# Performance work log

Measured on AMD Instinct MI355X. Metric: run time of the kernel, lower is better.

Reference implementation:

```python
import jax, jax.numpy as jnp
import numpy as np

DN = ('NCH', 'OIH', 'NCH')

def conv1d(x, w, b, pad):
    y = jax.lax.conv_general_dilated(x, w, (1,), [(pad, pad)], dimension_numbers=DN)
    return y if b is None else y + b[None, :, None]

def bn_eval(x, g, b, m, v, eps):
    s = g * jax.lax.rsqrt(v + eps)
    return x * s[None, :, None] + (b - m * s)[None, :, None]

def swish(x):
    return x * jax.nn.sigmoid(x)

def setup_inputs() -> dict:
    key = jax.random.key(0)
    ks = jax.random.split(key, 8)
    B, T, P = 16, 8192, 32
    inp = {
        'x': jax.random.normal(ks[0], (B, 1, T), jnp.float32),
        'conv_w': jax.random.normal(ks[1], (512, 1, 9), jnp.float32) * 0.1,
        'bn_g': jnp.ones((512,), jnp.float32),
        'bn_b': jnp.zeros((512,), jnp.float32),
        'bn_m': jnp.zeros((512,), jnp.float32),
        'bn_v': jnp.ones((512,), jnp.float32),
        'p1_w': jax.random.normal(ks[2], (P, 2, 31), jnp.float32) * 0.1,
        'p1_b': jnp.zeros((P,), jnp.float32),
        'pbn1_g': jnp.ones((P,), jnp.float32),
        'pbn1_b': jnp.zeros((P,), jnp.float32),
        'pbn1_m': jnp.zeros((P,), jnp.float32),
        'pbn1_v': jnp.ones((P,), jnp.float32),
        'p2_w': jax.random.normal(ks[3], (P, P, 15), jnp.float32) * 0.05,
        'p2_b': jnp.zeros((P,), jnp.float32),
        'pbn2_g': jnp.ones((P,), jnp.float32),
        'pbn2_b': jnp.zeros((P,), jnp.float32),
        'pbn2_m': jnp.zeros((P,), jnp.float32),
        'pbn2_v': jnp.ones((P,), jnp.float32),
        'p3_w': jax.random.normal(ks[4], (2, P, 15), jnp.float32) * 0.001,  # source scales last conv weight by 0.01
        'p3_b': jnp.full((2,), -np.log(2.0), jnp.float32),                 # source sets bias to -log(2)
        'norm_mean': jnp.ones((1,), jnp.float32),                           # eval-mode renorm buffer
    }
    return inp

def reference(x, conv_w, bn_g, bn_b, bn_m, bn_v,
              p1_w, p1_b, pbn1_g, pbn1_b, pbn1_m, pbn1_v,
              p2_w, p2_b, pbn2_g, pbn2_b, pbn2_m, pbn2_v,
              p3_w, p3_b, norm_mean):
    B, _, T = x.shape
    # main conv -> BN(eps=1e-3) -> GLU(dim=1); dropout is identity in eval
    h = conv1d(x, conv_w, None, 9 // 2)                 # [B, 512, T]
    h = bn_eval(h, bn_g, bn_b, bn_m, bn_v, 1e-3)
    a, g = jnp.split(h, 2, axis=1)
    features = a * jax.nn.sigmoid(g)                    # [B, 256, T]
    # predictor on cat([x, x*x])
    j = conv1d(jnp.concatenate([x, x * x], axis=1), p1_w, p1_b, 15)
    j = swish(bn_eval(j, pbn1_g, pbn1_b, pbn1_m, pbn1_v, 1e-5))
    j = conv1d(j, p2_w, p2_b, 7)
    j = swish(bn_eval(j, pbn2_g, pbn2_b, pbn2_m, pbn2_v, 1e-5))
    j = conv1d(j, p3_w, p3_b, 7)                        # [B, 2, T]
    weights = jax.nn.sigmoid(j[:, 0, :])                # [B, T]
    moves = jax.nn.sigmoid(j[:, 1, :])
    bmoves = moves
    moves = moves * norm_mean[0]                        # eval: renorm = norm_mean buffer
    # CIF-style dynamic pooling (row_pool), vectorized over batch
    feats = jnp.transpose(features, (0, 2, 1))          # [B, T, C]
    fw = feats * weights[..., None]
    poses = jnp.cumsum(jax.lax.stop_gradient(moves), axis=1)  # moves.detach() in source
    floors = jnp.floor(poses)
    w1 = 1.0 - (poses - floors)
    w2 = poses - floors
    fl = floors.astype(jnp.int32)
    ce = fl + 1
    Lmax = T + 2  # static bound: poses <= T so ceil index <= T+1
    C = fw.shape[2]
    def pool(fw_i, fl_i, ce_i, w1_i, w2_i):
        out = jnp.zeros((Lmax, C), fw_i.dtype)
        out = out.at[fl_i].add(w1_i[:, None] * fw_i)
        out = out.at[ce_i].add(w2_i[:, None] * fw_i)
        return out
    x_evs = jax.vmap(pool)(fw, fl, ce, w1, w2)          # [B, Lmax, C]
    lens = fl[:, -1] + 2                                 # int(ceils[-1]) + 1
    x_evs = jnp.transpose(x_evs, (0, 2, 1))             # [B, C, Lmax]
    pad = 3 - (Lmax % 3)
    x_evs = jnp.pad(x_evs, ((0, 0), (0, 0), (0, pad)))
    return x_evs, lens, bmoves, weights
```

## Files before the change

kernel.cpp:

```cpp
#include <hip/hip_runtime.h>
#include <math.h>

static constexpr int TT = 8192;
static constexpr int LFULL = 8196;
static constexpr int BSTRIDE = LFULL + 2;

static constexpr size_t XE_OFF   = 0;
static constexpr size_t LENS_OFF = (size_t)16*256*LFULL;
static constexpr size_t BM_OFF   = LENS_OFF + 16;
static constexpr size_t WT_OFF   = BM_OFF + (size_t)16*TT;

static constexpr size_t U_OFF     = 0;
static constexpr size_t V_OFF     = U_OFF + (size_t)16*32*TT;
static constexpr size_t MOVES_OFF = V_OFF + (size_t)16*32*TT;
static constexpr size_t C1_OFF    = MOVES_OFF + (size_t)16*TT;
static constexpr size_t C2_OFF    = C1_OFF + (size_t)16*TT;
static constexpr size_t BND_OFF   = U_OFF;

__device__ __forceinline__ float sig_(float z) { return 1.0f / (1.0f + __expf(-z)); }

__global__ __launch_bounds__(256) void k_conv1(
    const float* __restrict__ x,
    const float* __restrict__ p1w, const float* __restrict__ p1b,
    const float* __restrict__ g1, const float* __restrict__ b1,
    const float* __restrict__ m1, const float* __restrict__ v1,
    float* __restrict__ u)
{
    __shared__ float xin[2 * 320];
    __shared__ float w1t[2 * 992];
    const int tid = threadIdx.x;
    const int b = blockIdx.y;
    const int t0 = blockIdx.x * 256;

    for (int idx = tid; idx < 640; idx += 256) {
        int ci = idx / 320, xl = idx - ci * 320;
        int id = t0 - 15 + xl;
        float val = 0.f;
        if (xl < 286 && id >= 0 && id < TT) val = x[b * TT + id];
        xin[idx] = ci ? val * val : val;
    }
    for (int idx = tid; idx < 1984; idx += 256) {
        int c = idx / 62; int r = idx - c * 62; int ci = r / 31; int k = r - ci * 31;
        w1t[ci * 992 + c * 31 + k] = p1w[idx];
    }
    __syncthreads();

    const int tg = tid >> 5, c = tid & 31;
    float acc[32];
    const float bias = p1b[c];
#pragma unroll
    for (int i = 0; i < 32; ++i) acc[i] = bias;

    for (int h = 0; h < 4; ++h) {
        for (int ci = 0; ci < 2; ++ci) {
            float win[40];
            const float4* wp = (const float4*)(&xin[ci * 320 + tg * 32 + h * 8]);
#pragma unroll
            for (int r = 0; r < 10; ++r) {
                float4 q = wp[r];
                win[4*r] = q.x; win[4*r+1] = q.y; win[4*r+2] = q.z; win[4*r+3] = q.w;
            }
#pragma unroll
            for (int k = 0; k < 31; ++k) {
                float w = w1t[ci * 992 + c * 31 + k];
#pragma unroll
                for (int i = 0; i < 8; ++i) acc[h*8+i] = fmaf(w, win[i + k], acc[h*8+i]);
            }
        }
    }
    const float s = g1[c] * rsqrtf(v1[c] + 1e-5f);
    const float sh = b1[c] - m1[c] * s;
    float* up = &u[((size_t)(b * 32 + c)) * TT + t0 + tg * 32];
#pragma unroll
    for (int i = 0; i < 8; ++i) {
        float z0 = fmaf(acc[4*i+0], s, sh);
        float z1 = fmaf(acc[4*i+1], s, sh);
        float z2 = fmaf(acc[4*i+2], s, sh);
        float z3 = fmaf(acc[4*i+3], s, sh);
        ((float4*)up)[i] = make_float4(z0 * sig_(z0), z1 * sig_(z1), z2 * sig_(z2), z3 * sig_(z3));
    }
}

__global__ __launch_bounds__(256) void k_conv2(
    const float* __restrict__ u,
    const float* __restrict__ p2w, const float* __restrict__ p2b,
    const float* __restrict__ g2, const float* __restrict__ b2,
    const float* __restrict__ m2, const float* __restrict__ v2,
    float* __restrict__ vout)
{
    __shared__ float uld[32 * 144];
    __shared__ float w2t[32 * 240];
    const int tid = threadIdx.x;
    const int b = blockIdx.y;
    const int t0 = blockIdx.x * 128;
    const int ch = blockIdx.z;

    for (int idx = tid; idx < 32 * 144; idx += 256) {
        int ci = idx / 144, tl = idx - ci * 144;
        int tg = t0 - 7 + tl;
        float val = 0.f;
        if (tl < 142 && tg >= 0 && tg < TT) val = u[((size_t)(b * 32 + ci)) * TT + tg];
        uld[idx] = val;
    }
    for (int idx = tid; idx < 32 * 240; idx += 256) {
        int ci = idx / 240; int r = idx - ci * 240; int cl = r / 15; int k = r - cl * 15;
        w2t[idx] = p2w[(ch * 16 + cl) * 480 + ci * 15 + k];
    }
    __syncthreads();

    const int tg = tid >> 4, cl = tid & 15;
    const int c = ch * 16 + cl;
    float acc[8];
    const float bias = p2b[c];
#pragma unroll
    for (int i = 0; i < 8; ++i) acc[i] = bias;

    for (int ci = 0; ci < 32; ++ci) {
        float win[24];
        const float4* wp = (const float4*)(&uld[ci * 144 + tg * 8]);
#pragma unroll
        for (int r = 0; r < 6; ++r) {
            float4 q = wp[r];
            win[4*r] = q.x; win[4*r+1] = q.y; win[4*r+2] = q.z; win[4*r+3] = q.w;
        }
#pragma unroll
        for (int k = 0; k < 15; ++k) {
            float w = w2t[ci * 240 + cl * 15 + k];
#pragma unroll
            for (int i = 0; i < 8; ++i) acc[i] = fmaf(w, win[i + k], acc[i]);
        }
    }
    const float s = g2[c] * rsqrtf(v2[c] + 1e-5f);
    const float sh = b2[c] - m2[c] * s;
    float o[8];
#pragma unroll
    for (int i = 0; i < 8; ++i) { float z = fmaf(acc[i], s, sh); o[i] = z * sig_(z); }
    float* vp = &vout[((size_t)(b * 32 + c)) * TT + t0 + tg * 8];
    ((float4*)vp)[0] = make_float4(o[0], o[1], o[2], o[3]);
    ((float4*)vp)[1] = make_float4(o[4], o[5], o[6], o[7]);
}

__global__ __launch_bounds__(256) void k_conv3(
    const float* __restrict__ vin,
    const float* __restrict__ p3w, const float* __restrict__ p3b,
    const float* __restrict__ nm,
    float* __restrict__ outw, float* __restrict__ outbm, float* __restrict__ moves)
{
    __shared__ float vld[32 * 272];
    const int tid = threadIdx.x;
    const int b = blockIdx.y;
    const int t0 = blockIdx.x * 256;

    for (int idx = tid; idx < 32 * 272; idx += 256) {
        int ci = idx / 272, tl = idx - ci * 272;
        int tg = t0 - 7 + tl;
        float val = 0.f;
        if (tl < 270 && tg >= 0 && tg < TT) val = vin[((size_t)(b * 32 + ci)) * TT + tg];
        vld[idx] = val;
    }
    __syncthreads();

    float a0 = p3b[0], a1 = p3b[1];
    for (int ci = 0; ci < 32; ++ci) {
        float win[15];
#pragma unroll
        for (int k = 0; k < 15; ++k) win[k] = vld[ci * 272 + tid + k];
#pragma unroll
        for (int k = 0; k < 15; ++k) {
            a0 = fmaf(p3w[ci * 15 + k], win[k], a0);
            a1 = fmaf(p3w[480 + ci * 15 + k], win[k], a1);
        }
    }
    const int t = t0 + tid;
    const float wt = sig_(a0);
    const float bm = sig_(a1);
    outw[b * TT + t] = wt;
    outbm[b * TT + t] = bm;
    moves[b * TT + t] = bm * nm[0];
}

__global__ __launch_bounds__(1024) void k_scan(
    const float* __restrict__ moves, const float* __restrict__ wts,
    float* __restrict__ coef1, float* __restrict__ coef2,
    int* __restrict__ bnd, float* __restrict__ lens)
{
    __shared__ float wsum[16];
    const int tid = threadIdx.x;
    const int b = blockIdx.x;
    const int lane = tid & 63, wv = tid >> 6;
    float carry = 0.f;

    int* bb = &bnd[b * BSTRIDE];
    for (int i = tid; i < BSTRIDE; i += 1024) bb[i] = TT;
    if (tid == 0) { bb[0] = 0; bb[1] = 0; }
    __syncthreads();

    const float4* mv4 = (const float4*)&moves[b * TT];
    const float4* wt4 = (const float4*)&wts[b * TT];
    float4* c14 = (float4*)&coef1[b * TT];
    float4* c24 = (float4*)&coef2[b * TT];

    for (int chunk = 0; chunk < 2; ++chunk) {
        const int idx = chunk * 1024 + tid;
        float4 m = mv4[idx];
        const float s = m.x + m.y + m.z + m.w;
        float v = s;
#pragma unroll
        for (int off = 1; off < 64; off <<= 1) {
            float n = __shfl_up(v, off, 64);
            if (lane >= off) v += n;
        }
        if (lane == 63) wsum[wv] = v;
        __syncthreads();
        float pre = carry;
        for (int w = 0; w < wv; ++w) pre += wsum[w];
        float tot = 0.f;
#pragma unroll
        for (int w = 0; w < 16; ++w) tot += wsum[w];
        const float base = pre + (v - s);
        const float p0 = base + m.x;
        const float p1 = p0 + m.y;
        const float p2 = p1 + m.z;
        const float p3 = p2 + m.w;
        const float4 w4 = wt4[idx];
        const float fr0 = p0 - floorf(p0), fr1 = p1 - floorf(p1);
        const float fr2 = p2 - floorf(p2), fr3 = p3 - floorf(p3);
        c14[idx] = make_float4((1.f - fr0) * w4.x, (1.f - fr1) * w4.y,
                               (1.f - fr2) * w4.z, (1.f - fr3) * w4.w);
        c24[idx] = make_float4(fr0 * w4.x, fr1 * w4.y, fr2 * w4.z, fr3 * w4.w);
        {
            int lf = (int)floorf(base) + 1;
            const int lfe = (int)floorf(p3);
            const int tbase = idx << 2;
            for (; lf <= lfe; ++lf) {
                const float lff = (float)lf;
                int t = tbase;
                if (p0 >= lff) { }
                else if (p1 >= lff) t += 1;
                else if (p2 >= lff) t += 2;
                else t += 3;
                if (lf + 1 < BSTRIDE) bb[lf + 1] = t;
            }
        }
        if (chunk == 1 && tid == 1023) lens[b] = floorf(p3) + 2.0f;
        carry += tot;
        __syncthreads();
    }
}

static constexpr int LTILE = 16;
static constexpr int CHK = 128;

__global__ __launch_bounds__(256) void k_pool(
    const float* __restrict__ x,
    const float* __restrict__ cw,
    const float* __restrict__ bng, const float* __restrict__ bnb,
    const float* __restrict__ bnm, const float* __restrict__ bnv,
    const float* __restrict__ coef1, const float* __restrict__ coef2,
    const int* __restrict__ bnd,
    float* __restrict__ xevs)
{
    __shared__ float out_lds[256 * 17];
    __shared__ float4 xl4[36];
    __shared__ float4 c1l4[CHK / 4], c2l4[CHK / 4];
    __shared__ int lbs[LTILE + 2];
    float* xl = (float*)xl4;
    float* c1l = (float*)c1l4;
    float* c2l = (float*)c2l4;

    const int tid = threadIdx.x;
    const int b = blockIdx.y;
    const int l0 = blockIdx.x * LTILE;
    const int LTa = min(LTILE, LFULL - l0);

    if (tid < LTa + 2) lbs[tid] = bnd[b * BSTRIDE + l0 + tid];
    __syncthreads();

    const int t_lo = lbs[0];
    const int t_hi = lbs[LTa + 1];
    const size_t rowbase = (size_t)b * 256 * LFULL + l0;

    if (t_lo >= t_hi) {
        const float4 z = make_float4(0.f, 0.f, 0.f, 0.f);
#pragma unroll
        for (int it = 0; it < 4; ++it) {
            int idx4 = it * 256 + tid;
            int cc = idx4 >> 2, q = (idx4 & 3) << 2;
            if (q < LTa)
                *(float4*)(&xevs[rowbase + (size_t)cc * LFULL + q]) = z;
        }
        return;
    }

    {
#pragma unroll
        for (int li = 0; li < 17; ++li) out_lds[tid * 17 + li] = 0.f;
    }

    const int c = tid;
    float wa[9], wg[9];
#pragma unroll
    for (int k = 0; k < 9; ++k) { wa[k] = cw[c * 9 + k]; wg[k] = cw[(c + 256) * 9 + k]; }
    const float sa = bng[c] * rsqrtf(bnv[c] + 1e-3f);
    const float sha = bnb[c] - bnm[c] * sa;
    const float sg = bng[c + 256] * rsqrtf(bnv[c + 256] + 1e-3f);
    const float shg = bnb[c + 256] - bnm[c + 256] * sg;

    const float* xg = &x[b * TT];
    const float* c1g = &coef1[b * TT];
    const float* c2g = &coef2[b * TT];

    float accA = 0.f, accB = 0.f;
    int j = 0;
    int nb = lbs[1];

    for (int cs = t_lo; cs < t_hi; cs += CHK) {
        const int ce = min(cs + CHK, t_hi);
        const int len = ce - cs;
        __syncthreads();
        for (int idx = tid; idx < len + 12; idx += 256) {
            int id = cs - 4 + idx;
            xl[idx] = (id >= 0 && id < TT) ? xg[id] : 0.f;
        }
        if (tid < len) { c1l[tid] = c1g[cs + tid]; c2l[tid] = c2g[cs + tid]; }
        __syncthreads();

        const int len4 = len >> 2;
        for (int g = 0; g < len4; ++g) {
            float4 A = xl4[g], Bq = xl4[g + 1], Cq = xl4[g + 2];
            float w[12] = {A.x, A.y, A.z, A.w, Bq.x, Bq.y, Bq.z, Bq.w, Cq.x, Cq.y, Cq.z, Cq.w};
            float f[4];
#pragma unroll
            for (int i = 0; i < 4; ++i) {
                float s0 = 0.f, s1 = 0.f;
#pragma unroll
                for (int k = 0; k < 9; ++k) { s0 = fmaf(wa[k], w[i + k], s0); s1 = fmaf(wg[k], w[i + k], s1); }
                const float av = fmaf(s0, sa, sha);
                const float gv = fmaf(s1, sg, shg);
                f[i] = av * sig_(gv);
            }
            float4 c1v = c1l4[g], c2v = c2l4[g];
            const float c1a[4] = {c1v.x, c1v.y, c1v.z, c1v.w};
            const float c2a[4] = {c2v.x, c2v.y, c2v.z, c2v.w};
            const int tb = cs + (g << 2);
#pragma unroll
            for (int i = 0; i < 4; ++i) {
                const int t = tb + i;
                while (t >= nb) {
                    int li = j - 1;
                    if (li >= 0 && li < LTa) out_lds[c * 17 + li] = accA;
                    accA = accB; accB = 0.f;
                    ++j;
                    nb = lbs[j + 1];
                }
                accA = fmaf(c1a[i], f[i], accA);
                accB = fmaf(c2a[i], f[i], accB);
            }
        }
        for (int t = cs + (len4 << 2); t < ce; ++t) {
            const int il = t - cs;
            float s0 = 0.f, s1 = 0.f;
#pragma unroll
            for (int k = 0; k < 9; ++k) { float xv = xl[il + k]; s0 = fmaf(wa[k], xv, s0); s1 = fmaf(wg[k], xv, s1); }
            const float av = fmaf(s0, sa, sha);
            const float gv = fmaf(s1, sg, shg);
            const float f0 = av * sig_(gv);
            while (t >= nb) {
                int li = j - 1;
                if (li >= 0 && li < LTa) out_lds[c * 17 + li] = accA;
                accA = accB; accB = 0.f;
                ++j;
                nb = lbs[j + 1];
            }
            accA = fmaf(c1l[il], f0, accA);
            accB = fmaf(c2l[il], f0, accB);
        }
    }
    {
        int li = j - 1;
        if (li >= 0 && li < LTa) out_lds[c * 17 + li] = accA;
    }
    __syncthreads();

#pragma unroll
    for (int it = 0; it < 4; ++it) {
        int idx4 = it * 256 + tid;
        int cc = idx4 >> 2, q = (idx4 & 3) << 2;
        if (q < LTa) {
            float4 o;
            o.x = out_lds[cc * 17 + q + 0];
            o.y = out_lds[cc * 17 + q + 1];
            o.z = out_lds[cc * 17 + q + 2];
            o.w = out_lds[cc * 17 + q + 3];
            *(float4*)(&xevs[rowbase + (size_t)cc * LFULL + q]) = o;
        }
    }
}

extern "C" void kernel_launch(void* const* d_in, const int* in_sizes, int n_in,
                              void* d_out, int out_size, void* d_ws, size_t ws_size,
                              hipStream_t stream) {
    (void)in_sizes; (void)n_in; (void)out_size; (void)ws_size;
    const float* x      = (const float*)d_in[0];
    const float* conv_w = (const float*)d_in[1];
    const float* bn_g   = (const float*)d_in[2];
    const float* bn_b   = (const float*)d_in[3];
    const float* bn_m   = (const float*)d_in[4];
    const float* bn_v   = (const float*)d_in[5];
    const float* p1_w   = (const float*)d_in[6];
    const float* p1_b   = (const float*)d_in[7];
    const float* pbn1_g = (const float*)d_in[8];
    const float* pbn1_b = (const float*)d_in[9];
    const float* pbn1_m = (const float*)d_in[10];
    const float* pbn1_v = (const float*)d_in[11];
    const float* p2_w   = (const float*)d_in[12];
    const float* p2_b   = (const float*)d_in[13];
    const float* pbn2_g = (const float*)d_in[14];
    const float* pbn2_b = (const float*)d_in[15];
    const float* pbn2_m = (const float*)d_in[16];
    const float* pbn2_v = (const float*)d_in[17];
    const float* p3_w   = (const float*)d_in[18];
    const float* p3_b   = (const float*)d_in[19];
    const float* nm     = (const float*)d_in[20];

    float* out = (float*)d_out;
    float* ws  = (float*)d_ws;
    float* u     = ws + U_OFF;
    float* v     = ws + V_OFF;
    float* moves = ws + MOVES_OFF;
    float* coef1 = ws + C1_OFF;
    float* coef2 = ws + C2_OFF;
    int*   bnd   = (int*)(ws + BND_OFF);
    float* xevs  = out + XE_OFF;
    float* lens  = out + LENS_OFF;
    float* bmv   = out + BM_OFF;
    float* wts   = out + WT_OFF;

    k_conv1<<<dim3(32, 16), 256, 0, stream>>>(x, p1_w, p1_b, pbn1_g, pbn1_b, pbn1_m, pbn1_v, u);
    k_conv2<<<dim3(64, 16, 2), 256, 0, stream>>>(u, p2_w, p2_b, pbn2_g, pbn2_b, pbn2_m, pbn2_v, v);
    k_conv3<<<dim3(32, 16), 256, 0, stream>>>(v, p3_w, p3_b, nm, wts, bmv, moves);
    k_scan<<<16, 1024, 0, stream>>>(moves, wts, coef1, coef2, bnd, lens);
    k_pool<<<dim3((LFULL + LTILE - 1) / LTILE, 16), 256, 0, stream>>>(
        x, conv_w, bn_g, bn_b, bn_m, bn_v, coef1, coef2, bnd, xevs);
}
```

Baseline: 376.8 us.

## Split conv2 LDS staging into halves and move tail zeroing into a dedicated kernel

```diff
diff --git a/kernel.cpp b/kernel.cpp
--- a/kernel.cpp
+++ b/kernel.cpp
@@ -88,26 +88,13 @@
     const float* __restrict__ m2, const float* __restrict__ v2,
     float* __restrict__ vout)
 {
-    __shared__ float uld[32 * 144];
-    __shared__ float w2t[32 * 240];
+    __shared__ float uld[16 * 144];
+    __shared__ float w2t[16 * 240];
     const int tid = threadIdx.x;
     const int b = blockIdx.y;
     const int t0 = blockIdx.x * 128;
     const int ch = blockIdx.z;
 
-    for (int idx = tid; idx < 32 * 144; idx += 256) {
-        int ci = idx / 144, tl = idx - ci * 144;
-        int tg = t0 - 7 + tl;
-        float val = 0.f;
-        if (tl < 142 && tg >= 0 && tg < TT) val = u[((size_t)(b * 32 + ci)) * TT + tg];
-        uld[idx] = val;
-    }
-    for (int idx = tid; idx < 32 * 240; idx += 256) {
-        int ci = idx / 240; int r = idx - ci * 240; int cl = r / 15; int k = r - cl * 15;
-        w2t[idx] = p2w[(ch * 16 + cl) * 480 + ci * 15 + k];
-    }
-    __syncthreads();
-
     const int tg = tid >> 4, cl = tid & 15;
     const int c = ch * 16 + cl;
     float acc[8];
@@ -115,19 +102,35 @@
 #pragma unroll
     for (int i = 0; i < 8; ++i) acc[i] = bias;
 
-    for (int ci = 0; ci < 32; ++ci) {
-        float win[24];
-        const float4* wp = (const float4*)(&uld[ci * 144 + tg * 8]);
-#pragma unroll
-        for (int r = 0; r < 6; ++r) {
-            float4 q = wp[r];
-            win[4*r] = q.x; win[4*r+1] = q.y; win[4*r+2] = q.z; win[4*r+3] = q.w;
-        }
-#pragma unroll
-        for (int k = 0; k < 15; ++k) {
-            float w = w2t[ci * 240 + cl * 15 + k];
-#pragma unroll
-            for (int i = 0; i < 8; ++i) acc[i] = fmaf(w, win[i + k], acc[i]);
+    for (int h = 0; h < 2; ++h) {
+        __syncthreads();
+        for (int idx = tid; idx < 16 * 144; idx += 256) {
+            int ci = idx / 144, tl = idx - ci * 144;
+            int tgl = t0 - 7 + tl;
+            float val = 0.f;
+            if (tl < 142 && tgl >= 0 && tgl < TT) val = u[((size_t)(b * 32 + h * 16 + ci)) * TT + tgl];
+            uld[idx] = val;
+        }
+        for (int idx = tid; idx < 16 * 240; idx += 256) {
+            int ci = idx / 240; int r = idx - ci * 240; int cl2 = r / 15; int k = r - cl2 * 15;
+            w2t[idx] = p2w[(ch * 16 + cl2) * 480 + (h * 16 + ci) * 15 + k];
+        }
+        __syncthreads();
+
+        for (int ci = 0; ci < 16; ++ci) {
+            float win[24];
+            const float4* wp = (const float4*)(&uld[ci * 144 + tg * 8]);
+#pragma unroll
+            for (int r = 0; r < 6; ++r) {
+                float4 q = wp[r];
+                win[4*r] = q.x; win[4*r+1] = q.y; win[4*r+2] = q.z; win[4*r+3] = q.w;
+            }
+#pragma unroll
+            for (int k = 0; k < 15; ++k) {
+                float w = w2t[ci * 240 + cl * 15 + k];
+#pragma unroll
+                for (int i = 0; i < 8; ++i) acc[i] = fmaf(w, win[i + k], acc[i]);
+            }
         }
     }
     const float s = g2[c] * rsqrtf(v2[c] + 1e-5f);
@@ -248,6 +251,21 @@
     }
 }
 
+__global__ __launch_bounds__(256) void k_zero(
+    const float* __restrict__ lens, float* __restrict__ xevs)
+{
+    const int b = blockIdx.y;
+    const int cg = blockIdx.x;
+    const int zs = (((int)lens[b]) + 15) & ~15;
+    if (zs >= LFULL) return;
+    const int n4 = (LFULL - zs) >> 2;
+    const float4 z = make_float4(0.f, 0.f, 0.f, 0.f);
+    for (int r = 0; r < 16; ++r) {
+        float4* row4 = (float4*)&xevs[((size_t)(b * 256 + cg * 16 + r)) * LFULL + zs];
+        for (int i = threadIdx.x; i < n4; i += 256) row4[i] = z;
+    }
+}
+
 static constexpr int LTILE = 16;
 static constexpr int CHK = 128;
 
@@ -278,24 +296,12 @@
 
     const int t_lo = lbs[0];
     const int t_hi = lbs[LTa + 1];
+    if (t_lo >= t_hi) return;
+
     const size_t rowbase = (size_t)b * 256 * LFULL + l0;
 
-    if (t_lo >= t_hi) {
-        const float4 z = make_float4(0.f, 0.f, 0.f, 0.f);
-#pragma unroll
-        for (int it = 0; it < 4; ++it) {
-            int idx4 = it * 256 + tid;
-            int cc = idx4 >> 2, q = (idx4 & 3) << 2;
-            if (q < LTa)
-                *(float4*)(&xevs[rowbase + (size_t)cc * LFULL + q]) = z;
-        }
-        return;
-    }
-
-    {
-#pragma unroll
-        for (int li = 0; li < 17; ++li) out_lds[tid * 17 + li] = 0.f;
-    }
+#pragma unroll
+    for (int li = 0; li < 17; ++li) out_lds[tid * 17 + li] = 0.f;
 
     const int c = tid;
     float wa[9], wg[9];
@@ -440,6 +446,7 @@
     k_conv2<<<dim3(64, 16, 2), 256, 0, stream>>>(u, p2_w, p2_b, pbn2_g, pbn2_b, pbn2_m, pbn2_v, v);
     k_conv3<<<dim3(32, 16), 256, 0, stream>>>(v, p3_w, p3_b, nm, wts, bmv, moves);
     k_scan<<<16, 1024, 0, stream>>>(moves, wts, coef1, coef2, bnd, lens);
+    k_zero<<<dim3(16, 16), 256, 0, stream>>>(lens, xevs);
     k_pool<<<dim3((LFULL + LTILE - 1) / LTILE, 16), 256, 0, stream>>>(
         x, conv_w, bn_g, bn_b, bn_m, bn_v, coef1, coef2, bnd, xevs);
 }
```

After: 358.3 us. 1.05x faster.
